# Optimization experiments

Hardware: AMD Instinct MI355X
Metric: run time of the kernel (lower is better)

Reference implementation:

```python
import jax, jax.numpy as jnp
import numpy as np

D_MODEL = 1024
NUM_HEADS = 16
D_HEAD = D_MODEL // NUM_HEADS
MAX_DISTANCE = 128
SEQ_LEN = 2048


def setup_inputs() -> dict:
    key = jax.random.key(0)
    k_x, k_qkv, k_out, k_bias = jax.random.split(key, 4)
    scale = 1.0 / np.sqrt(D_MODEL)
    return {
        "x": jax.random.normal(k_x, (SEQ_LEN, D_MODEL), dtype=jnp.float32),
        "w_qkv": jax.random.normal(k_qkv, (D_MODEL, 3 * D_MODEL), dtype=jnp.float32) * scale,
        "w_out": jax.random.normal(k_out, (D_MODEL, D_MODEL), dtype=jnp.float32) * scale,
        "rel_bias": jax.random.normal(k_bias, (MAX_DISTANCE, NUM_HEADS), dtype=jnp.float32) * 0.02,
    }


def _position_bias(rel_bias, seq_len):
    # relative_position[q, k] = k - q; bucket = clip(|rel|, 0, max_distance-1)
    ctx = jnp.arange(seq_len)[:, None]
    mem = jnp.arange(seq_len)[None, :]
    bucket = jnp.clip(jnp.abs(mem - ctx), 0, MAX_DISTANCE - 1)  # [q, k]
    return rel_bias[bucket]  # [q, k, h]


def reference(x, w_qkv, w_out, rel_bias):
    seq_len = x.shape[0]
    qkv = x @ w_qkv  # [s, 3*d_model]
    q, k, v = jnp.split(qkv, 3, axis=-1)
    q = q.reshape(seq_len, NUM_HEADS, D_HEAD)
    k = k.reshape(seq_len, NUM_HEADS, D_HEAD)
    v = v.reshape(seq_len, NUM_HEADS, D_HEAD)
    bias = _position_bias(rel_bias, seq_len)  # [q, k, h]
    # flax dot_product_attention semantics: scale q by 1/sqrt(d_head), add bias, softmax over kv
    scores = jnp.einsum("qhd,khd->hqk", q, k) / jnp.sqrt(jnp.asarray(D_HEAD, q.dtype))
    scores = scores + jnp.transpose(bias, (2, 0, 1))  # [h, q, k]
    weights = jax.nn.softmax(scores, axis=-1)
    attn = jnp.einsum("hqk,khd->qhd", weights, v)  # [s, h, d_head]
    attn = attn.reshape(1, seq_len, D_MODEL)
    return attn @ w_out  # [1, s, d_model]
```

## Files before the change

kernel.cpp:

```cpp
#include <hip/hip_runtime.h>
#include <hip/hip_bf16.h>

#define SEQ   2048
#define DM    1024
#define NH    16
#define DH    64
#define MAXD  128

#define LOG2E 1.44269504f

typedef __attribute__((ext_vector_type(8))) short  short8;
typedef __attribute__((ext_vector_type(4))) float  float4v;

__device__ __forceinline__ short8 ld8(const void* p) {
    short8 v; __builtin_memcpy(&v, p, 16); return v;
}
__device__ __forceinline__ void st8(void* p, short8 v) {
    __builtin_memcpy(p, &v, 16);
}
__device__ __forceinline__ short bf16bits(float f) {
    __hip_bfloat16 b = __float2bfloat16(f);
    short s; __builtin_memcpy(&s, &b, 2); return s;
}
__device__ __forceinline__ short bf16fast(float f) {
    unsigned u = __builtin_bit_cast(unsigned, f);
    return (short)((u + 0x8000u) >> 16);
}
__device__ __forceinline__ float bits2f(short s) {
    unsigned u = (unsigned)(unsigned short)s << 16;
    return __builtin_bit_cast(float, u);
}
__device__ __forceinline__ float fexp2(float x) {
    float r; asm("v_exp_f32 %0, %1" : "=v"(r) : "v"(x)); return r;
}

__device__ __forceinline__ void async16(void* lds, const void* g) {
    __builtin_amdgcn_global_load_lds(
        (const __attribute__((address_space(1))) unsigned int*)g,
        (__attribute__((address_space(3))) unsigned int*)lds, 16, 0, 0);
}

template <int CTRL>
__device__ __forceinline__ float dppmov(float x) {
    return __builtin_bit_cast(float,
        __builtin_amdgcn_update_dpp(0, __builtin_bit_cast(int, x), CTRL, 0xf, 0xf, true));
}
__device__ __forceinline__ float red16max(float x) {
    x = fmaxf(x, dppmov<0xB1>(x));
    x = fmaxf(x, dppmov<0x4E>(x));
    x = fmaxf(x, dppmov<0x141>(x));
    x = fmaxf(x, dppmov<0x140>(x));
    return x;
}
__device__ __forceinline__ float red16sum(float x) {
    x += dppmov<0xB1>(x);
    x += dppmov<0x4E>(x);
    x += dppmov<0x141>(x);
    x += dppmov<0x140>(x);
    return x;
}

__global__ __launch_bounds__(256) void prep_kernel(
    const float* __restrict__ wq, const float* __restrict__ wo,
    const float* __restrict__ x,
    __hip_bfloat16* __restrict__ wqT, __hip_bfloat16* __restrict__ woT,
    __hip_bfloat16* __restrict__ xb) {
    const int t = threadIdx.x;
    const int bx = blockIdx.x;
    if (bx >= 128) {
        const size_t id = (size_t)(bx - 128) * 32 + blockIdx.y;
        const size_t i  = id * 2048 + t * 8;
        float f[8]; __builtin_memcpy(f, x + i, 32);
        short8 v;
#pragma unroll
        for (int j = 0; j < 8; ++j) v[j] = bf16bits(f[j]);
        st8(xb + i, v);
        return;
    }
    __shared__ __hip_bfloat16 tile[32][33];
    const int tx = t % 32, ty = t / 32;
    const int r0 = blockIdx.y * 32;
    const float* src; __hip_bfloat16* dst; int ss, ds, c0;
    if (bx < 96) { src = wq; dst = wqT; ss = 3 * DM; ds = DM; c0 = bx * 32; }
    else         { src = wo; dst = woT; ss = DM;     ds = DM; c0 = (bx - 96) * 32; }
#pragma unroll
    for (int i = 0; i < 4; ++i)
        tile[ty + i * 8][tx] = __float2bfloat16(src[(size_t)(r0 + ty + i * 8) * ss + c0 + tx]);
    __syncthreads();
#pragma unroll
    for (int i = 0; i < 4; ++i)
        dst[(size_t)(c0 + ty + i * 8) * ds + r0 + tx] = tile[tx][ty + i * 8];
}

__global__ __launch_bounds__(256) void gemm_qkv(
    const __hip_bfloat16* __restrict__ A,
    const __hip_bfloat16* __restrict__ BT,
    __hip_bfloat16* __restrict__ C,
    __hip_bfloat16* __restrict__ vTg,
    int M, int N, int K) {
    __shared__ short As[2 * 128 * 32];
    __shared__ short Bs[2 * 64 * 32];
    __shared__ short Tv[64 * 132];

    const int t = threadIdx.x;
    const int w = t >> 6, lane = t & 63;
    const int l15 = lane & 15, quad = lane >> 4;
    const int row0 = blockIdx.y * 128;
    const int col0 = blockIdx.x * 64;
    const int wm = w >> 1, wn = w & 1;

    float4v acc[4][2];
#pragma unroll
    for (int i = 0; i < 4; ++i)
#pragma unroll
        for (int j = 0; j < 2; ++j) acc[i][j] = (float4v){0.f, 0.f, 0.f, 0.f};

    const int mloc0 = lane >> 2;
    const int u     = lane & 3;

    for (int k0 = 0; k0 < K; k0 += 64) {
#pragma unroll
        for (int kc = 0; kc < 2; ++kc) {
#pragma unroll
            for (int i = 0; i < 2; ++i) {
                const int c = 2 * w + i;
                async16(&As[kc * 4096 + c * 512],
                        A + (size_t)(row0 + c * 16 + mloc0) * K + k0 + kc * 32 + u * 8);
            }
            async16(&Bs[kc * 2048 + w * 512],
                    BT + (size_t)(col0 + w * 16 + mloc0) * K + k0 + kc * 32 + u * 8);
        }
        __syncthreads();

#pragma unroll
        for (int kc = 0; kc < 2; ++kc) {
            short8 af[4], bf[2];
#pragma unroll
            for (int mt = 0; mt < 4; ++mt)
                af[mt] = ld8(&As[kc * 4096 + (wm * 64 + mt * 16 + l15) * 32 + quad * 8]);
#pragma unroll
            for (int nt = 0; nt < 2; ++nt)
                bf[nt] = ld8(&Bs[kc * 2048 + (wn * 32 + nt * 16 + l15) * 32 + quad * 8]);
#pragma unroll
            for (int mt = 0; mt < 4; ++mt)
#pragma unroll
                for (int nt = 0; nt < 2; ++nt)
                    acc[mt][nt] = __builtin_amdgcn_mfma_f32_16x16x32_bf16(
                        af[mt], bf[nt], acc[mt][nt], 0, 0, 0);
        }
        __syncthreads();
    }

    if (col0 < 2 * DM) {
#pragma unroll
        for (int mt = 0; mt < 4; ++mt)
#pragma unroll
            for (int nt = 0; nt < 2; ++nt)
#pragma unroll
                for (int r = 0; r < 4; ++r) {
                    const int row = row0 + wm * 64 + mt * 16 + quad * 4 + r;
                    const int col = col0 + wn * 32 + nt * 16 + l15;
                    C[(size_t)row * N + col] = __float2bfloat16(acc[mt][nt][r]);
                }
    } else {
#pragma unroll
        for (int mt = 0; mt < 4; ++mt)
#pragma unroll
            for (int nt = 0; nt < 2; ++nt)
#pragma unroll
                for (int r = 0; r < 4; ++r)
                    Tv[(wn * 32 + nt * 16 + l15) * 132 + wm * 64 + mt * 16 + quad * 4 + r] =
                        bf16bits(acc[mt][nt][r]);
        __syncthreads();
#pragma unroll
        for (int p = 0; p < 4; ++p) {
            const int idx = p * 256 + t;
            const int dl = idx >> 4, uu = idx & 15;
            st8(&vTg[((size_t)(col0 - 2 * DM) + dl) * SEQ + row0 + uu * 8],
                ld8(&Tv[dl * 132 + uu * 8]));
        }
    }
}

__global__ __launch_bounds__(256) void gemm_out(
    const __hip_bfloat16* __restrict__ A,
    const __hip_bfloat16* __restrict__ BT,
    float* __restrict__ C,
    int M, int N, int K) {
    __shared__ short As[2 * 64 * 32];
    __shared__ short Bs[2 * 64 * 32];

    const int t = threadIdx.x;
    const int w = t >> 6, lane = t & 63;
    const int l15 = lane & 15, quad = lane >> 4;
    const int row0 = blockIdx.y * 64;
    const int col0 = blockIdx.x * 64;
    const int wm = w >> 1, wn = w & 1;

    float4v acc[2][2];
#pragma unroll
    for (int i = 0; i < 2; ++i)
#pragma unroll
        for (int j = 0; j < 2; ++j) acc[i][j] = (float4v){0.f, 0.f, 0.f, 0.f};

    const int mloc0 = lane >> 2;
    const int u     = lane & 3;

    for (int k0 = 0; k0 < K; k0 += 64) {
#pragma unroll
        for (int kc = 0; kc < 2; ++kc) {
            async16(&As[kc * 2048 + w * 512],
                    A + (size_t)(row0 + w * 16 + mloc0) * K + k0 + kc * 32 + u * 8);
            async16(&Bs[kc * 2048 + w * 512],
                    BT + (size_t)(col0 + w * 16 + mloc0) * K + k0 + kc * 32 + u * 8);
        }
        __syncthreads();

#pragma unroll
        for (int kc = 0; kc < 2; ++kc) {
            short8 af[2], bf[2];
#pragma unroll
            for (int mt = 0; mt < 2; ++mt)
                af[mt] = ld8(&As[kc * 2048 + (wm * 32 + mt * 16 + l15) * 32 + quad * 8]);
#pragma unroll
            for (int nt = 0; nt < 2; ++nt)
                bf[nt] = ld8(&Bs[kc * 2048 + (wn * 32 + nt * 16 + l15) * 32 + quad * 8]);
#pragma unroll
            for (int mt = 0; mt < 2; ++mt)
#pragma unroll
                for (int nt = 0; nt < 2; ++nt)
                    acc[mt][nt] = __builtin_amdgcn_mfma_f32_16x16x32_bf16(
                        af[mt], bf[nt], acc[mt][nt], 0, 0, 0);
        }
        __syncthreads();
    }

#pragma unroll
    for (int mt = 0; mt < 2; ++mt)
#pragma unroll
        for (int nt = 0; nt < 2; ++nt)
#pragma unroll
            for (int r = 0; r < 4; ++r) {
                const int row = row0 + wm * 32 + mt * 16 + quad * 4 + r;
                const int col = col0 + wn * 32 + nt * 16 + l15;
                C[(size_t)row * N + col] = acc[mt][nt][r];
            }
}

#define TK  128
#define KS  68
#define VS  132

__global__ __launch_bounds__(256) void attn_mfma(
    const __hip_bfloat16* __restrict__ qkv,
    const __hip_bfloat16* __restrict__ vT,
    const float* __restrict__ rel_bias,
    __hip_bfloat16* __restrict__ attnb) {
    __shared__ short KtPl[TK * KS];
    __shared__ short Vt[DH * VS];
    __shared__ float biasL[MAXD];

    const int t = threadIdx.x;
    const int w = t >> 6, lane = t & 63;
    const int l15 = lane & 15, quad = lane >> 4;

    const int id = blockIdx.x;
    const int qb = (id >> 3) & 31;
    const int h  = (id & 7) + 8 * (id >> 8);
    const int q0 = qb * 64;
    const int qw = q0 + w * 16;

    if (t < MAXD) biasL[t] = rel_bias[t * NH + h] * LOG2E;

    short8 qf[2];
#pragma unroll
    for (int c = 0; c < 2; ++c) {
        short8 raw = ld8(qkv + (size_t)(qw + l15) * (3 * DM) + h * DH + c * 32 + quad * 8);
#pragma unroll
        for (int j = 0; j < 8; ++j) qf[c][j] = bf16bits(bits2f(raw[j]) * (0.125f * LOG2E));
    }

    float4v o_acc[4];
#pragma unroll
    for (int nt = 0; nt < 4; ++nt) o_acc[nt] = (float4v){0.f, 0.f, 0.f, 0.f};
    float m_i[4], l_i[4];
#pragma unroll
    for (int r = 0; r < 4; ++r) { m_i[r] = -1e30f; l_i[r] = 0.f; }

    for (int kb = 0; kb < SEQ / TK; ++kb) {
        const int k0 = kb * TK;
#pragma unroll
        for (int p = 0; p < 4; ++p) {
            const int idx = p * 256 + t;
            const int row = idx >> 3, u = idx & 7;
            st8(&KtPl[row * KS + u * 8],
                ld8(qkv + (size_t)(k0 + row) * (3 * DM) + DM + h * DH + u * 8));
        }
#pragma unroll
        for (int p = 0; p < 4; ++p) {
            const int idx = p * 256 + t;
            const int row = idx >> 4, u = idx & 15;
            st8(&Vt[row * VS + u * 8],
                ld8(vT + (size_t)(h * DH + row) * SEQ + k0 + u * 8));
        }
        __syncthreads();

        float4v s_acc[8];
#pragma unroll
        for (int kt = 0; kt < 8; ++kt) s_acc[kt] = (float4v){0.f, 0.f, 0.f, 0.f};
#pragma unroll
        for (int c = 0; c < 2; ++c)
#pragma unroll
            for (int kt = 0; kt < 8; ++kt) {
                short8 kf = ld8(&KtPl[(kt * 16 + l15) * KS + (c * 4 + quad) * 8]);
                s_acc[kt] = __builtin_amdgcn_mfma_f32_16x16x32_bf16(qf[c], kf, s_acc[kt], 0, 0, 0);
            }

        float sv[8][4];
        const int dlo = k0 - (qw + 15);
        const int dhi = qw - (k0 + TK - 1);
        if (dlo >= MAXD - 1 || dhi >= MAXD - 1) {
            const float bu = biasL[MAXD - 1];
#pragma unroll
            for (int kt = 0; kt < 8; ++kt)
#pragma unroll
                for (int r = 0; r < 4; ++r) sv[kt][r] = s_acc[kt][r] + bu;
        } else {
#pragma unroll
            for (int kt = 0; kt < 8; ++kt)
#pragma unroll
                for (int r = 0; r < 4; ++r) {
                    const int kg = k0 + kt * 16 + l15;
                    const int qg = qw + quad * 4 + r;
                    int rel = kg - qg; if (rel < 0) rel = -rel;
                    if (rel > MAXD - 1) rel = MAXD - 1;
                    sv[kt][r] = s_acc[kt][r] + biasL[rel];
                }
        }

        float rowm[4];
#pragma unroll
        for (int r = 0; r < 4; ++r) {
            float m = sv[0][r];
#pragma unroll
            for (int kt = 1; kt < 8; ++kt) m = fmaxf(m, sv[kt][r]);
            rowm[r] = red16max(m);
        }

        float al[4], rs[4];
#pragma unroll
        for (int r = 0; r < 4; ++r) {
            const float mn = fmaxf(m_i[r], rowm[r]);
            al[r] = fexp2(m_i[r] - mn);
            m_i[r] = mn;
            rs[r] = 0.f;
        }
#pragma unroll
        for (int kt = 0; kt < 8; ++kt)
#pragma unroll
            for (int r = 0; r < 4; ++r) {
                const float p = fexp2(sv[kt][r] - m_i[r]);
                sv[kt][r] = p;
                rs[r] += p;
            }
#pragma unroll
        for (int r = 0; r < 4; ++r) {
            rs[r] = red16sum(rs[r]);
            l_i[r] = l_i[r] * al[r] + rs[r];
        }
#pragma unroll
        for (int nt = 0; nt < 4; ++nt)
#pragma unroll
            for (int r = 0; r < 4; ++r) o_acc[nt][r] *= al[r];

        __syncthreads();

#pragma unroll
        for (int kt = 0; kt < 8; ++kt)
#pragma unroll
            for (int r = 0; r < 4; ++r)
                KtPl[w * 16 * VS + (quad * 4 + r) * VS + kt * 16 + l15] = bf16fast(sv[kt][r]);

#pragma unroll
        for (int kc = 0; kc < 4; ++kc) {
            short8 pf = ld8(&KtPl[w * 16 * VS + l15 * VS + kc * 32 + quad * 8]);
#pragma unroll
            for (int nt = 0; nt < 4; ++nt) {
                short8 vf = ld8(&Vt[(nt * 16 + l15) * VS + kc * 32 + quad * 8]);
                o_acc[nt] = __builtin_amdgcn_mfma_f32_16x16x32_bf16(pf, vf, o_acc[nt], 0, 0, 0);
            }
        }
        __syncthreads();
    }

#pragma unroll
    for (int nt = 0; nt < 4; ++nt)
#pragma unroll
        for (int r = 0; r < 4; ++r) {
            const int row = qw + quad * 4 + r;
            const int col = h * DH + nt * 16 + l15;
            attnb[(size_t)row * DM + col] = __float2bfloat16(o_acc[nt][r] / l_i[r]);
        }
}

extern "C" void kernel_launch(void* const* d_in, const int* in_sizes, int n_in,
                              void* d_out, int out_size, void* d_ws, size_t ws_size,
                              hipStream_t stream) {
    const float* x        = (const float*)d_in[0];
    const float* w_qkv    = (const float*)d_in[1];
    const float* w_out    = (const float*)d_in[2];
    const float* rel_bias = (const float*)d_in[3];
    float* out = (float*)d_out;

    char* p = (char*)d_ws;
    __hip_bfloat16* xb    = (__hip_bfloat16*)p;  p += (size_t)SEQ * DM * 2;
    __hip_bfloat16* wqT   = (__hip_bfloat16*)p;  p += (size_t)3 * DM * DM * 2;
    __hip_bfloat16* woT   = (__hip_bfloat16*)p;  p += (size_t)DM * DM * 2;
    __hip_bfloat16* qkvb  = (__hip_bfloat16*)p;  p += (size_t)SEQ * 3 * DM * 2;
    __hip_bfloat16* vT    = (__hip_bfloat16*)p;  p += (size_t)DM * SEQ * 2;
    __hip_bfloat16* attnb = (__hip_bfloat16*)p;

    prep_kernel<<<dim3(160, 32), 256, 0, stream>>>(w_qkv, w_out, x, wqT, woT, xb);

    gemm_qkv<<<dim3(3 * DM / 64, SEQ / 128), 256, 0, stream>>>(
        xb, wqT, qkvb, vT, SEQ, 3 * DM, DM);

    attn_mfma<<<512, 256, 0, stream>>>(qkvb, vT, rel_bias, attnb);

    gemm_out<<<dim3(DM / 64, SEQ / 64), 256, 0, stream>>>(
        attnb, woT, out, SEQ, DM, DM);
}
```

Measured before the change: 159.8 us.

## Double-buffer K/V tiles with async global-to-LDS loads and XOR swizzle

The attention kernel now streams K and V tiles straight into LDS with asynchronous global_load_lds. It double-buffers them so the next tile's load overlaps the current tile's QK^T, softmax and PV work, synchronised with explicit vmcnt waits and barriers. The key tile shrinks from 128 to 64, and the softmax probabilities move to their own per-wave LDS buffer instead of reusing the K buffer. An XOR swizzle on the global addresses replaces row padding to avoid LDS bank conflicts. The risks are more iterations with per-iteration barriers, and a final prefetch that reads one tile past the end of the K/V data.

```diff
diff --git a/kernel.cpp b/kernel.cpp
--- a/kernel.cpp
+++ b/kernel.cpp
@@ -39,6 +39,10 @@
         (const __attribute__((address_space(1))) unsigned int*)g,
         (__attribute__((address_space(3))) unsigned int*)lds, 16, 0, 0);
 }
+
+#define S_VMCNT(n) asm volatile("s_waitcnt vmcnt(" #n ")" ::: "memory")
+#define S_LGKM0()  asm volatile("s_waitcnt lgkmcnt(0)" ::: "memory")
+#define S_BAR()    __builtin_amdgcn_s_barrier()
 
 template <int CTRL>
 __device__ __forceinline__ float dppmov(float x) {
@@ -247,17 +251,18 @@
             }
 }
 
-#define TK  128
-#define KS  68
-#define VS  132
+#define TK   64
+#define NT   (SEQ / TK)
+#define PSTR 66
 
 __global__ __launch_bounds__(256) void attn_mfma(
     const __hip_bfloat16* __restrict__ qkv,
     const __hip_bfloat16* __restrict__ vT,
     const float* __restrict__ rel_bias,
     __hip_bfloat16* __restrict__ attnb) {
-    __shared__ short KtPl[TK * KS];
-    __shared__ short Vt[DH * VS];
+    __shared__ short Kt[2][TK * 64];
+    __shared__ short Vt[2][DH * TK];
+    __shared__ short Pl[4][16 * PSTR];
     __shared__ float biasL[MAXD];
 
     const int t = threadIdx.x;
@@ -280,6 +285,28 @@
         for (int j = 0; j < 8; ++j) qf[c][j] = bf16bits(bits2f(raw[j]) * (0.125f * LOG2E));
     }
 
+    const char* kp[2]; const char* vp[2];
+    {
+        const char* kqb = (const char*)qkv + (size_t)(DM + h * DH) * 2;
+        const char* vqb = (const char*)vT  + (size_t)(h * DH) * SEQ * 2;
+#pragma unroll
+        for (int r = 0; r < 2; ++r) {
+            const int o    = r * 4096 + w * 1024 + lane * 16;
+            const int row  = o >> 7, colb = o & 127;
+            const int sw   = (row & 7) << 4;
+            kp[r] = kqb + (size_t)row * (3 * DM * 2) + (colb ^ sw);
+            vp[r] = vqb + (size_t)row * (SEQ * 2)    + (colb ^ sw);
+        }
+    }
+    const int ldso = w * 512;
+
+#pragma unroll
+    for (int r = 0; r < 2; ++r) async16(&Kt[0][r * 2048 + ldso], kp[r]);
+#pragma unroll
+    for (int r = 0; r < 2; ++r) async16(&Vt[0][r * 2048 + ldso], vp[r]);
+#pragma unroll
+    for (int r = 0; r < 2; ++r) { kp[r] += (size_t)TK * 3 * DM * 2; vp[r] += TK * 2; }
+
     float4v o_acc[4];
 #pragma unroll
     for (int nt = 0; nt < 4; ++nt) o_acc[nt] = (float4v){0.f, 0.f, 0.f, 0.f};
@@ -287,47 +314,53 @@
 #pragma unroll
     for (int r = 0; r < 4; ++r) { m_i[r] = -1e30f; l_i[r] = 0.f; }
 
-    for (int kb = 0; kb < SEQ / TK; ++kb) {
-        const int k0 = kb * TK;
-#pragma unroll
-        for (int p = 0; p < 4; ++p) {
-            const int idx = p * 256 + t;
-            const int row = idx >> 3, u = idx & 7;
-            st8(&KtPl[row * KS + u * 8],
-                ld8(qkv + (size_t)(k0 + row) * (3 * DM) + DM + h * DH + u * 8));
-        }
-#pragma unroll
-        for (int p = 0; p < 4; ++p) {
-            const int idx = p * 256 + t;
-            const int row = idx >> 4, u = idx & 15;
-            st8(&Vt[row * VS + u * 8],
-                ld8(vT + (size_t)(h * DH + row) * SEQ + k0 + u * 8));
-        }
-        __syncthreads();
-
-        float4v s_acc[8];
-#pragma unroll
-        for (int kt = 0; kt < 8; ++kt) s_acc[kt] = (float4v){0.f, 0.f, 0.f, 0.f};
-#pragma unroll
-        for (int c = 0; c < 2; ++c)
-#pragma unroll
-            for (int kt = 0; kt < 8; ++kt) {
-                short8 kf = ld8(&KtPl[(kt * 16 + l15) * KS + (c * 4 + quad) * 8]);
-                s_acc[kt] = __builtin_amdgcn_mfma_f32_16x16x32_bf16(qf[c], kf, s_acc[kt], 0, 0, 0);
-            }
-
-        float sv[8][4];
+    const int swz = (l15 & 7) << 4;
+    const int ka0 = (l15 * 128 + ((quad * 16) ^ swz)) >> 1;
+    const int ka1 = (l15 * 128 + (((64) + quad * 16) ^ swz)) >> 1;
+
+    S_LGKM0();
+
+    for (int kb = 0; kb < NT; ++kb) {
+        const int k0  = kb * TK;
+        const int cur = kb & 1, nxt = cur ^ 1;
+
+#pragma unroll
+        for (int r = 0; r < 2; ++r) async16(&Kt[nxt][r * 2048 + ldso], kp[r]);
+#pragma unroll
+        for (int r = 0; r < 2; ++r) async16(&Vt[nxt][r * 2048 + ldso], vp[r]);
+#pragma unroll
+        for (int r = 0; r < 2; ++r) { kp[r] += (size_t)TK * 3 * DM * 2; vp[r] += TK * 2; }
+
+        S_VMCNT(4);
+        S_BAR();
+
+        float4v s_acc[4];
+#pragma unroll
+        for (int kt = 0; kt < 4; ++kt) s_acc[kt] = (float4v){0.f, 0.f, 0.f, 0.f};
+        const short* Kc = Kt[cur];
+#pragma unroll
+        for (int kt = 0; kt < 4; ++kt) {
+            short8 kf = ld8(Kc + kt * 1024 + ka0);
+            s_acc[kt] = __builtin_amdgcn_mfma_f32_16x16x32_bf16(qf[0], kf, s_acc[kt], 0, 0, 0);
+        }
+#pragma unroll
+        for (int kt = 0; kt < 4; ++kt) {
+            short8 kf = ld8(Kc + kt * 1024 + ka1);
+            s_acc[kt] = __builtin_amdgcn_mfma_f32_16x16x32_bf16(qf[1], kf, s_acc[kt], 0, 0, 0);
+        }
+
+        float sv[4][4];
         const int dlo = k0 - (qw + 15);
         const int dhi = qw - (k0 + TK - 1);
         if (dlo >= MAXD - 1 || dhi >= MAXD - 1) {
             const float bu = biasL[MAXD - 1];
 #pragma unroll
-            for (int kt = 0; kt < 8; ++kt)
+            for (int kt = 0; kt < 4; ++kt)
 #pragma unroll
                 for (int r = 0; r < 4; ++r) sv[kt][r] = s_acc[kt][r] + bu;
         } else {
 #pragma unroll
-            for (int kt = 0; kt < 8; ++kt)
+            for (int kt = 0; kt < 4; ++kt)
 #pragma unroll
                 for (int r = 0; r < 4; ++r) {
                     const int kg = k0 + kt * 16 + l15;
@@ -343,7 +376,7 @@
         for (int r = 0; r < 4; ++r) {
             float m = sv[0][r];
 #pragma unroll
-            for (int kt = 1; kt < 8; ++kt) m = fmaxf(m, sv[kt][r]);
+            for (int kt = 1; kt < 4; ++kt) m = fmaxf(m, sv[kt][r]);
             rowm[r] = red16max(m);
         }
 
@@ -356,7 +389,7 @@
             rs[r] = 0.f;
         }
 #pragma unroll
-        for (int kt = 0; kt < 8; ++kt)
+        for (int kt = 0; kt < 4; ++kt)
 #pragma unroll
             for (int r = 0; r < 4; ++r) {
                 const float p = fexp2(sv[kt][r] - m_i[r]);
@@ -373,25 +406,28 @@
 #pragma unroll
             for (int r = 0; r < 4; ++r) o_acc[nt][r] *= al[r];
 
-        __syncthreads();
-
-#pragma unroll
-        for (int kt = 0; kt < 8; ++kt)
+#pragma unroll
+        for (int kt = 0; kt < 4; ++kt)
 #pragma unroll
             for (int r = 0; r < 4; ++r)
-                KtPl[w * 16 * VS + (quad * 4 + r) * VS + kt * 16 + l15] = bf16fast(sv[kt][r]);
-
-#pragma unroll
-        for (int kc = 0; kc < 4; ++kc) {
-            short8 pf = ld8(&KtPl[w * 16 * VS + l15 * VS + kc * 32 + quad * 8]);
+                Pl[w][(quad * 4 + r) * PSTR + kt * 16 + l15] = bf16fast(sv[kt][r]);
+
+        const short* Vc = Vt[cur];
+#pragma unroll
+        for (int kc = 0; kc < 2; ++kc) {
+            short8 pf = ld8(&Pl[w][l15 * PSTR + kc * 32 + quad * 8]);
+            const int va = ((kc * 64 + quad * 16) ^ swz) >> 1;
 #pragma unroll
             for (int nt = 0; nt < 4; ++nt) {
-                short8 vf = ld8(&Vt[(nt * 16 + l15) * VS + kc * 32 + quad * 8]);
+                short8 vf = ld8(Vc + (nt * 16 + l15) * 64 + va);
                 o_acc[nt] = __builtin_amdgcn_mfma_f32_16x16x32_bf16(pf, vf, o_acc[nt], 0, 0, 0);
             }
         }
-        __syncthreads();
-    }
+
+        S_BAR();
+    }
+
+    S_VMCNT(0);
 
 #pragma unroll
     for (int nt = 0; nt < 4; ++nt)
```

After: 165.3 us. 1.03x slower.

## Prefetch next K/V tile into registers and give P its own LDS buffer

Applied to the files above, without the earlier changes.

The attention kernel now loads the next K and V tiles from global memory into registers while the current tile is being computed, then writes them to LDS at the top of the next iteration. P gets a dedicated per-wave LDS buffer instead of reusing the K tile area, which removes the barrier between the softmax and the P store. The remaining barriers use raw s_barrier with an explicit lgkmcnt wait. This raises register pressure and LDS use, which may lower occupancy.

```diff
diff --git a/kernel.cpp b/kernel.cpp
--- a/kernel.cpp
+++ b/kernel.cpp
@@ -39,6 +39,9 @@
         (const __attribute__((address_space(1))) unsigned int*)g,
         (__attribute__((address_space(3))) unsigned int*)lds, 16, 0, 0);
 }
+
+#define S_LGKM0()  asm volatile("s_waitcnt lgkmcnt(0)" ::: "memory")
+#define S_BAR()    __builtin_amdgcn_s_barrier()
 
 template <int CTRL>
 __device__ __forceinline__ float dppmov(float x) {
@@ -247,17 +250,19 @@
             }
 }
 
-#define TK  128
-#define KS  68
-#define VS  132
+#define TK    128
+#define NTILE (SEQ / TK)
+#define KS    68
+#define VS    132
 
 __global__ __launch_bounds__(256) void attn_mfma(
     const __hip_bfloat16* __restrict__ qkv,
     const __hip_bfloat16* __restrict__ vT,
     const float* __restrict__ rel_bias,
     __hip_bfloat16* __restrict__ attnb) {
-    __shared__ short KtPl[TK * KS];
+    __shared__ short Kt[TK * KS];
     __shared__ short Vt[DH * VS];
+    __shared__ short Pl[4][16 * VS];
     __shared__ float biasL[MAXD];
 
     const int t = threadIdx.x;
@@ -287,23 +292,47 @@
 #pragma unroll
     for (int r = 0; r < 4; ++r) { m_i[r] = -1e30f; l_i[r] = 0.f; }
 
-    for (int kb = 0; kb < SEQ / TK; ++kb) {
+    short8 pk[4], pv[4];
+#pragma unroll
+    for (int p = 0; p < 4; ++p) {
+        const int idx = p * 256 + t;
+        pk[p] = ld8(qkv + (size_t)(idx >> 3) * (3 * DM) + DM + h * DH + (idx & 7) * 8);
+    }
+#pragma unroll
+    for (int p = 0; p < 4; ++p) {
+        const int idx = p * 256 + t;
+        pv[p] = ld8(vT + (size_t)(h * DH + (idx >> 4)) * SEQ + (idx & 15) * 8);
+    }
+
+    for (int kb = 0; kb < NTILE; ++kb) {
         const int k0 = kb * TK;
+
 #pragma unroll
         for (int p = 0; p < 4; ++p) {
             const int idx = p * 256 + t;
-            const int row = idx >> 3, u = idx & 7;
-            st8(&KtPl[row * KS + u * 8],
-                ld8(qkv + (size_t)(k0 + row) * (3 * DM) + DM + h * DH + u * 8));
+            st8(&Kt[(idx >> 3) * KS + (idx & 7) * 8], pk[p]);
         }
 #pragma unroll
         for (int p = 0; p < 4; ++p) {
             const int idx = p * 256 + t;
-            const int row = idx >> 4, u = idx & 15;
-            st8(&Vt[row * VS + u * 8],
-                ld8(vT + (size_t)(h * DH + row) * SEQ + k0 + u * 8));
-        }
-        __syncthreads();
+            st8(&Vt[(idx >> 4) * VS + (idx & 15) * 8], pv[p]);
+        }
+        S_LGKM0();
+        S_BAR();
+
+        if (kb + 1 < NTILE) {
+            const int kn = k0 + TK;
+#pragma unroll
+            for (int p = 0; p < 4; ++p) {
+                const int idx = p * 256 + t;
+                pk[p] = ld8(qkv + (size_t)(kn + (idx >> 3)) * (3 * DM) + DM + h * DH + (idx & 7) * 8);
+            }
+#pragma unroll
+            for (int p = 0; p < 4; ++p) {
+                const int idx = p * 256 + t;
+                pv[p] = ld8(vT + (size_t)(h * DH + (idx >> 4)) * SEQ + kn + (idx & 15) * 8);
+            }
+        }
 
         float4v s_acc[8];
 #pragma unroll
@@ -312,7 +341,7 @@
         for (int c = 0; c < 2; ++c)
 #pragma unroll
             for (int kt = 0; kt < 8; ++kt) {
-                short8 kf = ld8(&KtPl[(kt * 16 + l15) * KS + (c * 4 + quad) * 8]);
+                short8 kf = ld8(&Kt[(kt * 16 + l15) * KS + (c * 4 + quad) * 8]);
                 s_acc[kt] = __builtin_amdgcn_mfma_f32_16x16x32_bf16(qf[c], kf, s_acc[kt], 0, 0, 0);
             }
 
@@ -373,24 +402,23 @@
 #pragma unroll
             for (int r = 0; r < 4; ++r) o_acc[nt][r] *= al[r];
 
-        __syncthreads();
-
 #pragma unroll
         for (int kt = 0; kt < 8; ++kt)
 #pragma unroll
             for (int r = 0; r < 4; ++r)
-                KtPl[w * 16 * VS + (quad * 4 + r) * VS + kt * 16 + l15] = bf16fast(sv[kt][r]);
+                Pl[w][(quad * 4 + r) * VS + kt * 16 + l15] = bf16fast(sv[kt][r]);
 
 #pragma unroll
         for (int kc = 0; kc < 4; ++kc) {
-            short8 pf = ld8(&KtPl[w * 16 * VS + l15 * VS + kc * 32 + quad * 8]);
+            short8 pf = ld8(&Pl[w][l15 * VS + kc * 32 + quad * 8]);
 #pragma unroll
             for (int nt = 0; nt < 4; ++nt) {
                 short8 vf = ld8(&Vt[(nt * 16 + l15) * VS + kc * 32 + quad * 8]);
                 o_acc[nt] = __builtin_amdgcn_mfma_f32_16x16x32_bf16(pf, vf, o_acc[nt], 0, 0, 0);
             }
         }
-        __syncthreads();
+
+        S_BAR();
     }
 
 #pragma unroll
```

Result: no change. 158.8 us (-0.7%).

## Split attention KV range across two blocks and merge with a combine kernel

Applied to the files above, without the earlier changes.

Each attention block now processes only half of the key/value sequence, doubling the grid from 512 to 1024 blocks. Each half writes its normalized partial output in fp16 plus its running max and sum. A new combine kernel merges the two halves with log-sum-exp weights into the bf16 attention buffer. This aims to raise occupancy and parallelism on the many-CU GPU, at the cost of an extra launch, extra global traffic for the partials, and reuse of workspace that earlier kernels already consumed.

```diff
diff --git a/kernel.cpp b/kernel.cpp
--- a/kernel.cpp
+++ b/kernel.cpp
@@ -29,6 +29,12 @@
 __device__ __forceinline__ float bits2f(short s) {
     unsigned u = (unsigned)(unsigned short)s << 16;
     return __builtin_bit_cast(float, u);
+}
+__device__ __forceinline__ short fp16bits(float f) {
+    _Float16 h = (_Float16)f; short s; __builtin_memcpy(&s, &h, 2); return s;
+}
+__device__ __forceinline__ float f16tof(short s) {
+    _Float16 h; __builtin_memcpy(&h, &s, 2); return (float)h;
 }
 __device__ __forceinline__ float fexp2(float x) {
     float r; asm("v_exp_f32 %0, %1" : "=v"(r) : "v"(x)); return r;
@@ -247,15 +253,17 @@
             }
 }
 
-#define TK  128
-#define KS  68
-#define VS  132
-
-__global__ __launch_bounds__(256) void attn_mfma(
+#define TK    128
+#define NTILE (SEQ / 2 / TK)
+#define KS    68
+#define VS    132
+
+__global__ __launch_bounds__(256) void attn_part(
     const __hip_bfloat16* __restrict__ qkv,
     const __hip_bfloat16* __restrict__ vT,
     const float* __restrict__ rel_bias,
-    __hip_bfloat16* __restrict__ attnb) {
+    short* __restrict__ opart,
+    float* __restrict__ ml) {
     __shared__ short KtPl[TK * KS];
     __shared__ short Vt[DH * VS];
     __shared__ float biasL[MAXD];
@@ -266,7 +274,10 @@
 
     const int id = blockIdx.x;
     const int qb = (id >> 3) & 31;
-    const int h  = (id & 7) + 8 * (id >> 8);
+    const int c  = (id & 7) + 8 * (id >> 8);
+    const int h  = c & 15;
+    const int half = c >> 4;
+    const int kbase = half * (SEQ / 2);
     const int q0 = qb * 64;
     const int qw = q0 + w * 16;
 
@@ -274,10 +285,10 @@
 
     short8 qf[2];
 #pragma unroll
-    for (int c = 0; c < 2; ++c) {
-        short8 raw = ld8(qkv + (size_t)(qw + l15) * (3 * DM) + h * DH + c * 32 + quad * 8);
-#pragma unroll
-        for (int j = 0; j < 8; ++j) qf[c][j] = bf16bits(bits2f(raw[j]) * (0.125f * LOG2E));
+    for (int cc = 0; cc < 2; ++cc) {
+        short8 raw = ld8(qkv + (size_t)(qw + l15) * (3 * DM) + h * DH + cc * 32 + quad * 8);
+#pragma unroll
+        for (int j = 0; j < 8; ++j) qf[cc][j] = bf16bits(bits2f(raw[j]) * (0.125f * LOG2E));
     }
 
     float4v o_acc[4];
@@ -287,8 +298,8 @@
 #pragma unroll
     for (int r = 0; r < 4; ++r) { m_i[r] = -1e30f; l_i[r] = 0.f; }
 
-    for (int kb = 0; kb < SEQ / TK; ++kb) {
-        const int k0 = kb * TK;
+    for (int kb = 0; kb < NTILE; ++kb) {
+        const int k0 = kbase + kb * TK;
 #pragma unroll
         for (int p = 0; p < 4; ++p) {
             const int idx = p * 256 + t;
@@ -309,11 +320,11 @@
 #pragma unroll
         for (int kt = 0; kt < 8; ++kt) s_acc[kt] = (float4v){0.f, 0.f, 0.f, 0.f};
 #pragma unroll
-        for (int c = 0; c < 2; ++c)
+        for (int cc = 0; cc < 2; ++cc)
 #pragma unroll
             for (int kt = 0; kt < 8; ++kt) {
-                short8 kf = ld8(&KtPl[(kt * 16 + l15) * KS + (c * 4 + quad) * 8]);
-                s_acc[kt] = __builtin_amdgcn_mfma_f32_16x16x32_bf16(qf[c], kf, s_acc[kt], 0, 0, 0);
+                short8 kf = ld8(&KtPl[(kt * 16 + l15) * KS + (cc * 4 + quad) * 8]);
+                s_acc[kt] = __builtin_amdgcn_mfma_f32_16x16x32_bf16(qf[cc], kf, s_acc[kt], 0, 0, 0);
             }
 
         float sv[8][4];
@@ -399,8 +410,45 @@
         for (int r = 0; r < 4; ++r) {
             const int row = qw + quad * 4 + r;
             const int col = h * DH + nt * 16 + l15;
-            attnb[(size_t)row * DM + col] = __float2bfloat16(o_acc[nt][r] / l_i[r]);
-        }
+            opart[((size_t)half * SEQ + row) * DM + col] = fp16bits(o_acc[nt][r] / l_i[r]);
+        }
+    if (l15 == 0) {
+#pragma unroll
+        for (int r = 0; r < 4; ++r) {
+            const int row = qw + quad * 4 + r;
+            float* mp = ml + (((size_t)half * SEQ + row) * NH + h) * 2;
+            mp[0] = m_i[r];
+            mp[1] = l_i[r];
+        }
+    }
+}
+
+__global__ __launch_bounds__(256) void combine_kernel(
+    const short* __restrict__ opart,
+    const float* __restrict__ ml,
+    __hip_bfloat16* __restrict__ attnb) {
+    const size_t e = ((size_t)blockIdx.x * 256 + threadIdx.x) * 8;
+    const int row = (int)(e >> 10);
+    const int c0  = (int)(e & 1023);
+    const int h   = c0 >> 6;
+
+    const float* mp1 = ml + ((size_t)row * NH + h) * 2;
+    const float* mp2 = mp1 + (size_t)SEQ * NH * 2;
+    const float m1 = mp1[0], l1 = mp1[1];
+    const float m2 = mp2[0], l2 = mp2[1];
+    const float mx = fmaxf(m1, m2);
+    const float e1 = fexp2(m1 - mx) * l1;
+    const float e2 = fexp2(m2 - mx) * l2;
+    const float inv = 1.f / (e1 + e2);
+    const float w1 = e1 * inv, w2 = e2 * inv;
+
+    short8 a = ld8(opart + (size_t)row * DM + c0);
+    short8 b = ld8(opart + (size_t)SEQ * DM + (size_t)row * DM + c0);
+    short8 o;
+#pragma unroll
+    for (int j = 0; j < 8; ++j)
+        o[j] = bf16bits(w1 * f16tof(a[j]) + w2 * f16tof(b[j]));
+    st8(attnb + (size_t)row * DM + c0, o);
 }
 
 extern "C" void kernel_launch(void* const* d_in, const int* in_sizes, int n_in,
@@ -420,12 +468,16 @@
     __hip_bfloat16* vT    = (__hip_bfloat16*)p;  p += (size_t)DM * SEQ * 2;
     __hip_bfloat16* attnb = (__hip_bfloat16*)p;
 
+    short* opart = (short*)d_ws;
+    float* ml    = (float*)((char*)d_ws + (size_t)2 * SEQ * DM * 2);
+
     prep_kernel<<<dim3(160, 32), 256, 0, stream>>>(w_qkv, w_out, x, wqT, woT, xb);
 
     gemm_qkv<<<dim3(3 * DM / 64, SEQ / 128), 256, 0, stream>>>(
         xb, wqT, qkvb, vT, SEQ, 3 * DM, DM);
 
-    attn_mfma<<<512, 256, 0, stream>>>(qkvb, vT, rel_bias, attnb);
+    attn_part<<<1024, 256, 0, stream>>>(qkvb, vT, rel_bias, opart, ml);
+    combine_kernel<<<1024, 256, 0, stream>>>(opart, ml, attnb);
 
     gemm_out<<<dim3(DM / 64, SEQ / 64), 256, 0, stream>>>(
         attnb, woT, out, SEQ, DM, DM);
```

Measured after the change: 167.6 us. +4.9%, slower.
